# Kernel optimization log

Measured on AMD Instinct MI355X. Metric: run time of the kernel, lower is better.

The kernel has to match this reference:

```python
import jax, jax.numpy as jnp
import numpy as np
from jax import lax


def _ramp_filter_real(size):
    # torch ramp_filter: spatial-domain ramp, FFT is purely real (even symmetric)
    image_n = np.concatenate([np.arange(1, size // 2 + 1, 2),
                              np.arange(size // 2 - 1, 0, -2)]).astype(np.float64)
    f = np.zeros(size, dtype=np.float64)
    f[0] = 0.25
    f[1::2] = -1.0 / (np.pi * image_n) ** 2
    return (2.0 * np.real(np.fft.fft(f))).astype(np.float32)  # [size]


def setup_inputs() -> dict:
    key = jax.random.key(0)
    # sinogram: [B, C, detector_bins, n_angles]
    x = jax.random.normal(key, (4, 1, 512, 180), dtype=jnp.float32)
    return {"x": x}


def reference(x):
    B, C, S, A = x.shape  # S = in_size = it_size (circle=True), A = n_angles
    # ---- ramp filtering along detector axis (axis=2) ----
    pad_to = max(64, 1 << int(np.ceil(np.log2(2 * S))))
    xp = jnp.pad(x, ((0, 0), (0, 0), (0, pad_to - S), (0, 0)))
    ramp = jnp.asarray(_ramp_filter_real(pad_to))
    # original multiplies by complex filter r*(1+i); imag part of ifft is 0 for real x,
    # so real part equals standard ramp filtering
    Xf = jnp.fft.fft(xp, axis=2)
    filt = (ramp * (1.0 + 1.0j)).astype(jnp.complex64)
    xfilt = jnp.real(jnp.fft.ifft(Xf * filt[None, None, :, None], axis=2))
    xfilt = xfilt[:, :, :S, :].astype(x.dtype)  # [B,C,S,A]

    # ---- backprojection ----
    unit = jnp.linspace(-1.0, 1.0, S, dtype=x.dtype)
    ygrid, xgrid = jnp.meshgrid(unit, unit, indexing="ij")  # torch.meshgrid 'ij'
    thetas = (jnp.arange(A, dtype=x.dtype) * (np.pi / 180.0)).astype(x.dtype)
    # t coordinate in [-sqrt2, sqrt2]: [A,S,S]
    t = (xgrid[None] * jnp.cos(thetas)[:, None, None]
         - ygrid[None] * jnp.sin(thetas)[:, None, None])
    # grid_sample bilinear, align_corners=True, zeros padding; X coord selects angle i exactly
    p = (t + 1.0) * 0.5 * (S - 1)
    p0 = jnp.floor(p)
    w = (p - p0).astype(x.dtype)
    i0 = p0.astype(jnp.int32)
    i1 = i0 + 1
    v0 = ((i0 >= 0) & (i0 < S)).astype(x.dtype)
    v1 = ((i1 >= 0) & (i1 < S)).astype(x.dtype)
    i0c = jnp.clip(i0, 0, S - 1)
    i1c = jnp.clip(i1, 0, S - 1)

    xa = jnp.moveaxis(xfilt, 3, 0)  # [A,B,C,S]

    def body(acc, inp):
        xa_a, i0a, i1a, wa, v0a, v1a = inp
        g = (xa_a[:, :, i0a] * v0a * (1.0 - wa)
             + xa_a[:, :, i1a] * v1a * wa)  # [B,C,S,S]
        return acc + g, None

    reco0 = jnp.zeros((B, C, S, S), dtype=x.dtype)
    reco, _ = lax.scan(body, reco0, (xa, i0c, i1c, w, v0, v1))

    # circle mask + normalization
    mask = (xgrid ** 2 + ygrid ** 2) <= 1.0
    reco = jnp.where(mask[None, None], reco, 0.0)
    reco = reco * (np.pi / (2.0 * A))
    return reco
```

## Files before the change

### kernel.cpp

```cpp
#include <hip/hip_runtime.h>
#include <math.h>

namespace {

constexpr int BB  = 4;
constexpr int SS  = 512;
constexpr int AA  = 180;
constexpr int PAD = 112;
constexpr int RB  = SS + 2 * PAD;

typedef float v2f __attribute__((ext_vector_type(2)));

__global__ __launch_bounds__(256) void ramp_zero_kernel(
    const float* __restrict__ x, float* __restrict__ xf, float* __restrict__ out) {
  const int t = threadIdx.x;
  {
    const int bid = blockIdx.y * 90 + blockIdx.x;
    float4 z = make_float4(0.f, 0.f, 0.f, 0.f);
    for (int i = bid * 256 + t; i < (BB * SS * SS) / 4; i += 360 * 256)
      ((float4*)out)[i] = z;
  }

  __shared__ __align__(16) float xs[2][2][256];
  __shared__ __align__(16) float G[2][528];
  const int a0 = blockIdx.x * 2;
  const int b  = blockIdx.y;

  const float s  = (float)(M_PI / 360.0);
  const float cc = (float)(-2.0 / (M_PI * M_PI)) * s;
  for (int i = t; i < 528; i += 256) {
    { int kk = i;     float d = (float)(2 * kk - 511); G[0][i] = (kk < 512) ? cc / (d * d) : 0.0f; }
    { int kk = i + 1; float d = (float)(2 * kk - 511); G[1][i] = (kk < 512) ? cc / (d * d) : 0.0f; }
  }

  const float* xb = x + (size_t)b * (SS * AA) + a0;
  {
    int m = t;
    float2 v = *(const float2*)(xb + (size_t)m * AA);
    xs[0][m & 1][m >> 1] = v.x;  xs[1][m & 1][m >> 1] = v.y;
    m = t + 256;
    float2 v2 = *(const float2*)(xb + (size_t)m * AA);
    xs[0][m & 1][m >> 1] = v2.x; xs[1][m & 1][m >> 1] = v2.y;
  }
  __syncthreads();

  const int col = t >> 7;
  const int p   = (t >> 6) & 1;
  const int idx = t & 63;
  const float* Gp = G[p];
  const float* xv = xs[col][1 - p];

  float acc[4] = {0.f, 0.f, 0.f, 0.f};
  float W[8];
  {
    const int A0 = 4 * idx + 252;
    float4 w0 = *(const float4*)(Gp + A0);
    float4 w1 = *(const float4*)(Gp + A0 + 4);
    W[0] = w0.x; W[1] = w0.y; W[2] = w0.z; W[3] = w0.w;
    W[4] = w1.x; W[5] = w1.y; W[6] = w1.z; W[7] = w1.w;
  }

#pragma unroll
  for (int q = 0; q < 64; ++q) {
    const float4 xq = *(const float4*)(xv + 4 * q);
    float4 nw;
    if (q != 63) nw = *(const float4*)(Gp + (4 * idx + 252 - 4 * (q + 1)));
#pragma unroll
    for (int r = 0; r < 4; ++r) {
      acc[r] = fmaf(W[3 + r], xq.x, acc[r]);
      acc[r] = fmaf(W[2 + r], xq.y, acc[r]);
      acc[r] = fmaf(W[1 + r], xq.z, acc[r]);
      acc[r] = fmaf(W[0 + r], xq.w, acc[r]);
    }
    if (q != 63) {
      W[7] = W[3]; W[6] = W[2]; W[5] = W[1]; W[4] = W[0];
      W[0] = nw.x; W[1] = nw.y; W[2] = nw.z; W[3] = nw.w;
    }
  }

  const float selfc = 0.5f * s;
  const float* xsp = xs[col][p];
  float* orow = xf + ((size_t)(b * AA + a0 + col)) * SS;
#pragma unroll
  for (int r = 0; r < 4; ++r)
    orow[p + 8 * idx + 2 * r] = fmaf(selfc, xsp[4 * idx + r], acc[r]);
}

__global__ __launch_bounds__(256, 4) void backproject_kernel(
    const float* __restrict__ xf, float* __restrict__ out) {
  __shared__ __align__(16) v2f P[2][3][RB];
  __shared__ float2 trig[45];

  const int t     = threadIdx.x;
  const int w     = t >> 6;
  const int lane  = t & 63;
  const int tx    = blockIdx.x;
  const int ty    = blockIdx.y;
  const int b     = blockIdx.z >> 2;
  const int chunk = blockIdx.z & 3;
  const int a0    = chunk * 45;

  for (int i = t; i < 2 * 3 * 2 * PAD; i += 256) {
    int bu  = i / 672;
    int rem = i - bu * 672;
    int rr  = rem / 224;
    int o   = rem - rr * 224;
    int j   = (o < PAD) ? o : (o + SS);
    P[bu][rr][j] = (v2f){0.f, 0.f};
  }
  if (t < 45) {
    float th = (float)(a0 + t) * (float)(M_PI / 180.0);
    float sn, cn;
    sincosf(th, &sn, &cn);
    trig[t] = make_float2(cn * 255.5f, sn * 255.5f);
  }

  const float* src = xf + ((size_t)b * AA + a0) * SS;

  float2 fw[3], rv[3];
  auto ld = [&](int g) {
    const float* base = src + (size_t)(g * 3) * SS;
#pragma unroll
    for (int k = 0; k < 3; ++k) {
      const float* row = base + k * SS;
      fw[k] = *(const float2*)(row + 2 * t);
      rv[k] = *(const float2*)(row + 510 - 2 * t);
    }
  };
  auto st = [&](int buf) {
#pragma unroll
    for (int k = 0; k < 3; ++k) {
      float4 q = make_float4(fw[k].x, rv[k].y, fw[k].y, rv[k].x);
      *(float4*)&P[buf][k][PAD + 2 * t] = q;
    }
  };

  const int gx = tx * 64 + lane;
  const float step = 2.0f / 511.0f;
  const float xg = __fadd_rn(-1.0f, __fmul_rn((float)gx, step));
  float dy[8];
#pragma unroll
  for (int kk = 0; kk < 8; ++kk) {
    int gy = ty * 32 + w + 4 * kk;
    dy[kk] = -__fadd_rn(-1.0f, __fmul_rn((float)gy, step));
  }

  const float Kp = 255.5f + (float)PAD;
  v2f acc[8];
#pragma unroll
  for (int kk = 0; kk < 8; ++kk) acc[kk] = (v2f){0.f, 0.f};

  ld(0);
  st(0);
  __syncthreads();

  int buf = 0;
  for (int g = 0; g < 15; ++g) {
    if (g + 1 < 15) ld(g + 1);
#pragma unroll
    for (int aa = 0; aa < 3; ++aa) {
      const float2 cs = trig[g * 3 + aa];
      const float base = fmaf(xg, cs.x, Kp);
      const v2f* R = P[buf][aa];
#pragma unroll
      for (int kk = 0; kk < 8; ++kk) {
        float p = fmaf(dy[kk], cs.y, base);
        int   I = (int)p;
#if __has_builtin(__builtin_amdgcn_fractf)
        float wq = __builtin_amdgcn_fractf(p);
#else
        float wq = p - floorf(p);
#endif
        struct { v2f a, b; } q;
        __builtin_memcpy(&q, R + I, 16);
        v2f d  = q.b - q.a;
        v2f wv = {wq, wq};
        acc[kk] = (acc[kk] + q.a) + wv * d;
      }
    }
    if (g + 1 < 15) {
      st(buf ^ 1);
      __syncthreads();
      buf ^= 1;
    }
  }

  const int gxm  = 511 - gx;
  const float xgm = __fadd_rn(-1.0f, __fmul_rn((float)gxm, step));
  const float xx  = __fmul_rn(xg, xg);
  const float xxm = __fmul_rn(xgm, xgm);
#pragma unroll
  for (int kk = 0; kk < 8; ++kk) {
    int gy  = ty * 32 + w + 4 * kk;
    float yg = -dy[kk];
    float s0 = __fadd_rn(xx, __fmul_rn(yg, yg));
    if (s0 <= 1.0f)
      unsafeAtomicAdd(&out[((size_t)b * SS + gy) * SS + gx], acc[kk].x);
    int gym = 511 - gy;
    float ygm = __fadd_rn(-1.0f, __fmul_rn((float)gym, step));
    float s1 = __fadd_rn(xxm, __fmul_rn(ygm, ygm));
    if (s1 <= 1.0f)
      unsafeAtomicAdd(&out[((size_t)b * SS + gym) * SS + gxm], acc[kk].y);
  }
}

}

extern "C" void kernel_launch(void* const* d_in, const int* in_sizes, int n_in,
                              void* d_out, int out_size, void* d_ws, size_t ws_size,
                              hipStream_t stream) {
  const float* x   = (const float*)d_in[0];
  float*       out = (float*)d_out;
  float*       xf  = (float*)d_ws;

  ramp_zero_kernel<<<dim3(AA / 2, BB), 256, 0, stream>>>(x, xf, out);
  backproject_kernel<<<dim3(4, 16, 16), 256, 0, stream>>>(xf, out);
}
```

Before: 99.86 us.

## Cull out-of-circle backprojection tiles, shrink tiles and single-buffer LDS

Before any work, each backprojection block now checks whether its 64x16 pixel tile lies entirely outside the unit circle and returns early if so. The mirrored pixel each thread also writes has the same distance from the centre, so only masked-out output is skipped. Tile height is halved and the grid doubled. LDS goes from double- to single-buffered with an extra barrier, and the occupancy hint rises from 4 to 8 blocks per CU. The aim is to drop work on masked corners and raise occupancy, at the cost of losing load/compute overlap through the added sync.

```diff
diff --git a/kernel.cpp b/kernel.cpp
--- a/kernel.cpp
+++ b/kernel.cpp
@@ -86,9 +86,9 @@
     orow[p + 8 * idx + 2 * r] = fmaf(selfc, xsp[4 * idx + r], acc[r]);
 }
 
-__global__ __launch_bounds__(256, 4) void backproject_kernel(
+__global__ __launch_bounds__(256, 8) void backproject_kernel(
     const float* __restrict__ xf, float* __restrict__ out) {
-  __shared__ __align__(16) v2f P[2][3][RB];
+  __shared__ __align__(16) v2f P[3][RB];
   __shared__ float2 trig[45];
 
   const int t     = threadIdx.x;
@@ -100,13 +100,20 @@
   const int chunk = blockIdx.z & 3;
   const int a0    = chunk * 45;
 
-  for (int i = t; i < 2 * 3 * 2 * PAD; i += 256) {
-    int bu  = i / 672;
-    int rem = i - bu * 672;
-    int rr  = rem / 224;
-    int o   = rem - rr * 224;
-    int j   = (o < PAD) ? o : (o + SS);
-    P[bu][rr][j] = (v2f){0.f, 0.f};
+  {
+    const float step = 2.0f / 511.0f;
+    float x0 = -1.0f + (float)(tx * 64) * step, x1 = -1.0f + (float)(tx * 64 + 63) * step;
+    float y0 = -1.0f + (float)(ty * 16) * step, y1 = -1.0f + (float)(ty * 16 + 15) * step;
+    float mx = (x0 <= 0.f && x1 >= 0.f) ? 0.f : fminf(fabsf(x0), fabsf(x1));
+    float my = (y0 <= 0.f && y1 >= 0.f) ? 0.f : fminf(fabsf(y0), fabsf(y1));
+    if (mx * mx + my * my > 1.0f) return;
+  }
+
+  for (int i = t; i < 3 * 2 * PAD; i += 256) {
+    int rr = i / 224;
+    int o  = i - rr * 224;
+    int j  = (o < PAD) ? o : (o + SS);
+    P[rr][j] = (v2f){0.f, 0.f};
   }
   if (t < 45) {
     float th = (float)(a0 + t) * (float)(M_PI / 180.0);
@@ -127,43 +134,43 @@
       rv[k] = *(const float2*)(row + 510 - 2 * t);
     }
   };
-  auto st = [&](int buf) {
+  auto st = [&]() {
 #pragma unroll
     for (int k = 0; k < 3; ++k) {
       float4 q = make_float4(fw[k].x, rv[k].y, fw[k].y, rv[k].x);
-      *(float4*)&P[buf][k][PAD + 2 * t] = q;
+      *(float4*)&P[k][PAD + 2 * t] = q;
     }
   };
 
   const int gx = tx * 64 + lane;
   const float step = 2.0f / 511.0f;
   const float xg = __fadd_rn(-1.0f, __fmul_rn((float)gx, step));
-  float dy[8];
-#pragma unroll
-  for (int kk = 0; kk < 8; ++kk) {
-    int gy = ty * 32 + w + 4 * kk;
+  float dy[4];
+#pragma unroll
+  for (int kk = 0; kk < 4; ++kk) {
+    int gy = ty * 16 + w + 4 * kk;
     dy[kk] = -__fadd_rn(-1.0f, __fmul_rn((float)gy, step));
   }
 
   const float Kp = 255.5f + (float)PAD;
-  v2f acc[8];
-#pragma unroll
-  for (int kk = 0; kk < 8; ++kk) acc[kk] = (v2f){0.f, 0.f};
+  v2f acc[4];
+#pragma unroll
+  for (int kk = 0; kk < 4; ++kk) acc[kk] = (v2f){0.f, 0.f};
 
   ld(0);
-  st(0);
+  st();
   __syncthreads();
 
-  int buf = 0;
   for (int g = 0; g < 15; ++g) {
-    if (g + 1 < 15) ld(g + 1);
+    const bool more = (g + 1 < 15);
+    if (more) ld(g + 1);
 #pragma unroll
     for (int aa = 0; aa < 3; ++aa) {
       const float2 cs = trig[g * 3 + aa];
       const float base = fmaf(xg, cs.x, Kp);
-      const v2f* R = P[buf][aa];
-#pragma unroll
-      for (int kk = 0; kk < 8; ++kk) {
+      const v2f* R = P[aa];
+#pragma unroll
+      for (int kk = 0; kk < 4; ++kk) {
         float p = fmaf(dy[kk], cs.y, base);
         int   I = (int)p;
 #if __has_builtin(__builtin_amdgcn_fractf)
@@ -178,10 +185,10 @@
         acc[kk] = (acc[kk] + q.a) + wv * d;
       }
     }
-    if (g + 1 < 15) {
-      st(buf ^ 1);
+    if (more) {
       __syncthreads();
-      buf ^= 1;
+      st();
+      __syncthreads();
     }
   }
 
@@ -190,8 +197,8 @@
   const float xx  = __fmul_rn(xg, xg);
   const float xxm = __fmul_rn(xgm, xgm);
 #pragma unroll
-  for (int kk = 0; kk < 8; ++kk) {
-    int gy  = ty * 32 + w + 4 * kk;
+  for (int kk = 0; kk < 4; ++kk) {
+    int gy  = ty * 16 + w + 4 * kk;
     float yg = -dy[kk];
     float s0 = __fadd_rn(xx, __fmul_rn(yg, yg));
     if (s0 <= 1.0f)
@@ -214,5 +221,5 @@
   float*       xf  = (float*)d_ws;
 
   ramp_zero_kernel<<<dim3(AA / 2, BB), 256, 0, stream>>>(x, xf, out);
-  backproject_kernel<<<dim3(4, 16, 16), 256, 0, stream>>>(xf, out);
-}
+  backproject_kernel<<<dim3(4, 32, 16), 256, 0, stream>>>(xf, out);
+}
```

Result: no change. 100.4 us (+0.5%).
